# Optimization experiments

Hardware: AMD Instinct MI355X
Metric: run time of the kernel (lower is better)

## Reference

```python
import jax, jax.numpy as jnp
import numpy as np

N_NODES = 100000
N_EDGES = 3200000
BATCH = 16
LAYER_NUMBER = 4


def setup_inputs() -> dict:
    key = jax.random.key(0)
    k1, k2, k3, k4 = jax.random.split(key, 4)
    x = jax.random.normal(k1, (N_NODES, BATCH), dtype=jnp.float32)
    # learnable per-edge weights (log1p(counts) at init in the original; the
    # parameter itself is what is learned, so a plain random init is faithful)
    weights = jax.random.normal(k2, (N_EDGES,), dtype=jnp.float32)
    row = jax.random.randint(k3, (N_EDGES,), 0, N_NODES, dtype=jnp.int64)
    col = jax.random.randint(k4, (N_EDGES,), 0, N_NODES, dtype=jnp.int64)
    return {"x": x, "weights": weights, "row": row, "col": col}


def reference(x, weights, row, col):
    # Repeated sparse COO SpMM: y <- A @ y, applied layer_number times,
    # where A[row[e], col[e]] = weights[e].
    def step(y, _):
        msg = weights[:, None] * y[col]                      # [E, B] gather + scale
        y_new = jax.ops.segment_sum(msg, row, num_segments=N_NODES)  # [N, B] scatter-add
        return y_new, None

    y, _ = jax.lax.scan(step, x, None, length=LAYER_NUMBER)
    return y
```

## Files before the change

kernel.cpp:

```cpp
#include <hip/hip_runtime.h>

#define N_NODES 100000
#define N_EDGES 3200000
#define BATCH 16
#define BKT_SHIFT 6
#define BKT_NODES 64
#define K_BUCKETS 1563
#define NB 512
#define SUB (N_EDGES / NB)
#define FT 512
#define CAP 4096
#define DONE_CTR 1600
#define FLAG_CTR 1601


__global__ void zero_kernel(int* __restrict__ totals, int* __restrict__ cursor) {
    int t = threadIdx.x;
    for (int k = t; k < 2048; k += 256) totals[k] = 0;
    for (int k = t; k < K_BUCKETS; k += 256) cursor[k] = 0;
}

__global__ void __launch_bounds__(FT, 4) build_kernel(
        const int* __restrict__ row, const int* __restrict__ col,
        const float* __restrict__ w,
        int* __restrict__ totals, int* __restrict__ bptr,
        int* __restrict__ row_ptr, int* __restrict__ cursor,
        uint2* __restrict__ entries) {
    __shared__ uint2 sbuf[SUB];
    __shared__ int lbeg[K_BUCKETS];
    __shared__ int lcur[K_BUCKETS];
    __shared__ int cross[FT / 64];
    __shared__ int crossg[FT / 64];
    __shared__ int lastflag;
    int t = threadIdx.x, blk = blockIdx.x;
    int lane = t & 63, wv = t >> 6;
    int base = blk * SUB;

    for (int k = t; k < K_BUCKETS; k += FT) lcur[k] = 0;
    __syncthreads();
    for (int e = base + t; e < base + SUB; e += FT)
        atomicAdd(&lcur[row[e] >> BKT_SHIFT], 1);
    __syncthreads();

    {
        int sink = 0;
        for (int k = t; k < K_BUCKETS; k += FT) {
            int v = lcur[k];
            if (v) sink += atomicAdd(&totals[k], v);
        }
        asm volatile("" :: "v"(sink));
    }
    __syncthreads();
    if (t == 0) {
        int old = atomicAdd(&totals[DONE_CTR], 1);
        lastflag = (old == (int)gridDim.x - 1);
    }
    __syncthreads();

    if (lastflag) {
        int gloc[4];
        int gsum = 0;
        #pragma unroll
        for (int i = 0; i < 4; i++) {
            int idx = t * 4 + i;
            int v = (idx < K_BUCKETS) ? atomicAdd(&totals[idx], 0) : 0;
            gloc[i] = v;
            gsum += v;
        }
        int gpref = gsum;
        #pragma unroll
        for (int off = 1; off < 64; off <<= 1) {
            int u = __shfl_up(gpref, off, 64);
            if (lane >= off) gpref += u;
        }
        if (lane == 63) crossg[wv] = gpref;
        __syncthreads();
        int gwbase = 0;
        for (int i = 0; i < wv; i++) gwbase += crossg[i];
        int gexcl = gwbase + gpref - gsum;
        int sink = 0;
        #pragma unroll
        for (int i = 0; i < 4; i++) {
            int idx = t * 4 + i;
            if (idx < K_BUCKETS) sink += atomicExch(&bptr[idx], gexcl);
            gexcl += gloc[i];
        }
        asm volatile("" :: "v"(sink));
        __syncthreads();
        if (t == 0) {
            bptr[K_BUCKETS] = N_EDGES;
            row_ptr[N_NODES] = N_EDGES;
            int o = atomicExch(&totals[FLAG_CTR], 1);
            asm volatile("" :: "v"(o));
        }
    }

    {
        int loc[4];
        int sum = 0;
        #pragma unroll
        for (int j = 0; j < 4; j++) {
            int k = t * 4 + j;
            int v = (k < K_BUCKETS) ? lcur[k] : 0;
            loc[j] = v;
            sum += v;
        }
        int pref = sum;
        #pragma unroll
        for (int off = 1; off < 64; off <<= 1) {
            int u = __shfl_up(pref, off, 64);
            if (lane >= off) pref += u;
        }
        if (lane == 63) cross[wv] = pref;
        __syncthreads();
        int wbase = 0;
        for (int i = 0; i < wv; i++) wbase += cross[i];
        int excl = wbase + pref - sum;
        #pragma unroll
        for (int j = 0; j < 4; j++) {
            int k = t * 4 + j;
            if (k < K_BUCKETS) { lbeg[k] = excl; lcur[k] = excl; }
            excl += loc[j];
        }
    }
    __syncthreads();

    for (int e = base + t; e < base + SUB; e += FT) {
        int r = row[e];
        int bkt = r >> BKT_SHIFT;
        int pos = atomicAdd(&lcur[bkt], 1);
        sbuf[pos] = make_uint2(((unsigned)(r & (BKT_NODES - 1)) << 17) | (unsigned)col[e],
                               __float_as_uint(w[e]));
    }
    __syncthreads();

    if (!lastflag) {
        if (t == 0)
            while (atomicAdd(&totals[FLAG_CTR], 0) == 0)
                __builtin_amdgcn_s_sleep(8);
        __syncthreads();
    }

    int lane4 = t & 3;
    int sgbase = lane & ~3;
    for (int k = (t >> 2); k < K_BUCKETS; k += FT / 4) {
        int lb = lbeg[k];
        int le = lcur[k];
        int cnt = le - lb;
        int d0 = 0;
        if (lane4 == 0 && cnt > 0)
            d0 = atomicAdd(&bptr[k], 0) + atomicAdd(&cursor[k], cnt);
        d0 = __shfl(d0, sgbase, 64);
        for (int i = lb + lane4; i < le; i += 4)
            entries[d0 + (i - lb)] = sbuf[i];
    }
}

__global__ void __launch_bounds__(256) nodesort_pull1_kernel(
        const int* __restrict__ bptr, uint2* __restrict__ entries,
        int* __restrict__ row_ptr,
        const float* __restrict__ x, float* __restrict__ out) {
    __shared__ uint2 ebuf[CAP];
    __shared__ int nh[BKT_NODES];
    __shared__ int nc[BKT_NODES];
    __shared__ int nstart[BKT_NODES + 1];
    int t = threadIdx.x, b = blockIdx.x;
    int beg = bptr[b], end = bptr[b + 1];
    int n = min(end - beg, CAP);
    if (t < BKT_NODES) nh[t] = 0;
    __syncthreads();
    uint2 rs[16];
    int cnt = 0;
    #pragma unroll
    for (int i = 0; i < 16; i++) {
        int k = t + i * 256;
        if (k < n) {
            uint2 r = entries[beg + k];
            rs[i] = r;
            atomicAdd(&nh[r.x >> 17], 1);
            cnt = i + 1;
        }
    }
    __syncthreads();
    if (t < BKT_NODES) {
        int v = nh[t];
        int pref = v;
        #pragma unroll
        for (int off = 1; off < BKT_NODES; off <<= 1) {
            int u = __shfl_up(pref, off, 64);
            if (t >= off) pref += u;
        }
        int excl = pref - v;
        nstart[t] = excl;
        nc[t] = excl;
        if (t == BKT_NODES - 1) nstart[BKT_NODES] = pref;
        int node = b * BKT_NODES + t;
        if (node < N_NODES) row_ptr[node] = beg + excl;
    }
    __syncthreads();
    #pragma unroll
    for (int i = 0; i < 16; i++) {
        if (i < cnt) {
            uint2 r = rs[i];
            int pos = atomicAdd(&nc[r.x >> 17], 1);
            ebuf[pos] = r;
            entries[beg + pos] = r;
        }
    }
    __syncthreads();
    int ln = t >> 2, q = t & 3;
    int node = b * BKT_NODES + ln;
    if (node >= N_NODES) return;
    int s = nstart[ln], e = nstart[ln + 1];
    float4 acc = make_float4(0.f, 0.f, 0.f, 0.f);
    int i = s;
    while (i + 8 <= e) {
        uint2 r0 = ebuf[i + 0], r1 = ebuf[i + 1], r2 = ebuf[i + 2], r3 = ebuf[i + 3];
        uint2 r4 = ebuf[i + 4], r5 = ebuf[i + 5], r6 = ebuf[i + 6], r7 = ebuf[i + 7];
        float4 y0 = *(const float4*)&x[(r0.x & 0x1FFFFu) * BATCH + q * 4];
        float4 y1 = *(const float4*)&x[(r1.x & 0x1FFFFu) * BATCH + q * 4];
        float4 y2 = *(const float4*)&x[(r2.x & 0x1FFFFu) * BATCH + q * 4];
        float4 y3 = *(const float4*)&x[(r3.x & 0x1FFFFu) * BATCH + q * 4];
        float4 y4 = *(const float4*)&x[(r4.x & 0x1FFFFu) * BATCH + q * 4];
        float4 y5 = *(const float4*)&x[(r5.x & 0x1FFFFu) * BATCH + q * 4];
        float4 y6 = *(const float4*)&x[(r6.x & 0x1FFFFu) * BATCH + q * 4];
        float4 y7 = *(const float4*)&x[(r7.x & 0x1FFFFu) * BATCH + q * 4];
        float w0 = __uint_as_float(r0.y), w1 = __uint_as_float(r1.y);
        float w2 = __uint_as_float(r2.y), w3 = __uint_as_float(r3.y);
        float w4 = __uint_as_float(r4.y), w5 = __uint_as_float(r5.y);
        float w6 = __uint_as_float(r6.y), w7 = __uint_as_float(r7.y);
        acc.x += w0 * y0.x; acc.y += w0 * y0.y; acc.z += w0 * y0.z; acc.w += w0 * y0.w;
        acc.x += w1 * y1.x; acc.y += w1 * y1.y; acc.z += w1 * y1.z; acc.w += w1 * y1.w;
        acc.x += w2 * y2.x; acc.y += w2 * y2.y; acc.z += w2 * y2.z; acc.w += w2 * y2.w;
        acc.x += w3 * y3.x; acc.y += w3 * y3.y; acc.z += w3 * y3.z; acc.w += w3 * y3.w;
        acc.x += w4 * y4.x; acc.y += w4 * y4.y; acc.z += w4 * y4.z; acc.w += w4 * y4.w;
        acc.x += w5 * y5.x; acc.y += w5 * y5.y; acc.z += w5 * y5.z; acc.w += w5 * y5.w;
        acc.x += w6 * y6.x; acc.y += w6 * y6.y; acc.z += w6 * y6.z; acc.w += w6 * y6.w;
        acc.x += w7 * y7.x; acc.y += w7 * y7.y; acc.z += w7 * y7.z; acc.w += w7 * y7.w;
        i += 8;
    }
    for (; i < e; i++) {
        uint2 r = ebuf[i];
        float4 yv = *(const float4*)&x[(r.x & 0x1FFFFu) * BATCH + q * 4];
        float wj = __uint_as_float(r.y);
        acc.x += wj * yv.x; acc.y += wj * yv.y;
        acc.z += wj * yv.z; acc.w += wj * yv.w;
    }
    *(float4*)&out[node * BATCH + q * 4] = acc;
}

__global__ void __launch_bounds__(256) pull_kernel(const float* __restrict__ y,
                            const uint2* __restrict__ entries,
                            const int* __restrict__ row_ptr,
                            float* __restrict__ out) {
    int tid = blockIdx.x * blockDim.x + threadIdx.x;
    int node = tid >> 2;
    int q = tid & 3;
    if (node >= N_NODES) return;
    int beg = row_ptr[node];
    int end = row_ptr[node + 1];
    float4 acc = make_float4(0.f, 0.f, 0.f, 0.f);
    if (beg < end) {
        int lim = end - 1;
        uint2 r[8];
        #pragma unroll
        for (int j = 0; j < 8; j++) r[j] = entries[min(beg + j, lim)];
        int i = beg;
        while (i + 8 <= end) {
            float4 yv[8];
            #pragma unroll
            for (int j = 0; j < 8; j++)
                yv[j] = *(const float4*)&y[(r[j].x & 0x1FFFFu) * BATCH + q * 4];
            uint2 nx[8];
            #pragma unroll
            for (int j = 0; j < 8; j++)
                nx[j] = entries[min(i + 8 + j, lim)];
            #pragma unroll
            for (int j = 0; j < 8; j++) {
                float wj = __uint_as_float(r[j].y);
                acc.x += wj * yv[j].x;
                acc.y += wj * yv[j].y;
                acc.z += wj * yv[j].z;
                acc.w += wj * yv[j].w;
            }
            #pragma unroll
            for (int j = 0; j < 8; j++) r[j] = nx[j];
            i += 8;
        }
        if (i < end) {
            float4 yv[8];
            #pragma unroll
            for (int j = 0; j < 8; j++)
                yv[j] = *(const float4*)&y[(r[j].x & 0x1FFFFu) * BATCH + q * 4];
            #pragma unroll
            for (int j = 0; j < 8; j++)
                if (i + j < end) {
                    float wj = __uint_as_float(r[j].y);
                    acc.x += wj * yv[j].x;
                    acc.y += wj * yv[j].y;
                    acc.z += wj * yv[j].z;
                    acc.w += wj * yv[j].w;
                }
        }
    }
    *(float4*)&out[node * BATCH + q * 4] = acc;
}

extern "C" void kernel_launch(void* const* d_in, const int* in_sizes, int n_in,
                              void* d_out, int out_size, void* d_ws, size_t ws_size,
                              hipStream_t stream) {
    const float* x   = (const float*)d_in[0];
    const float* w   = (const float*)d_in[1];
    const int*   row = (const int*)d_in[2];
    const int*   col = (const int*)d_in[3];
    float*       out = (float*)d_out;

    char* p = (char*)d_ws;
    uint2* entries = (uint2*)p;  p += (size_t)N_EDGES * sizeof(uint2);
    float* buf     = (float*)p;  p += (size_t)N_NODES * BATCH * sizeof(float);
    int* totals  = (int*)p;      p += 8192;
    int* bptr    = (int*)p;      p += 8192;
    int* cursor  = (int*)p;      p += 8192;
    int* row_ptr = (int*)p;

    zero_kernel<<<1, 256, 0, stream>>>(totals, cursor);
    build_kernel<<<NB, FT, 0, stream>>>(row, col, w, totals, bptr, row_ptr,
                                        cursor, entries);

    nodesort_pull1_kernel<<<K_BUCKETS, 256, 0, stream>>>(bptr, entries, row_ptr, x, buf);
    const int pgrid = (N_NODES * 4 + 255) / 256;
    pull_kernel<<<pgrid, 256, 0, stream>>>(buf, entries, row_ptr, out);
    pull_kernel<<<pgrid, 256, 0, stream>>>(out, entries, row_ptr, buf);
    pull_kernel<<<pgrid, 256, 0, stream>>>(buf, entries, row_ptr, out);
}
```

Baseline: 309.8 us.

## Fuse three pull SpMM layers into one persistent kernel with grid barriers

Replaces the three back-to-back pull_kernel launches with a single mega_pull_kernel that runs all three layers. Between layers it uses a global atomic-counter barrier, and it writes intermediates with system-coherent (sc0 sc1) stores so other XCDs can see them. The row pointers are loaded once and reused across layers. This is meant to remove two launch gaps and the kernel-boundary drains. In exchange it relies on all 1563 blocks being co-resident, adds spin-wait barrier overhead, and needs an extra workspace buffer, with a fallback to the old path if the workspace is too small.

```diff
diff --git a/kernel.cpp b/kernel.cpp
--- a/kernel.cpp
+++ b/kernel.cpp
@@ -12,6 +12,10 @@
 #define CAP 4096
 #define DONE_CTR 1600
 #define FLAG_CTR 1601
+#define PULL_CTR 1700
+#define PGRID 1563
+
+typedef float v4f __attribute__((ext_vector_type(4)));
 
 
 __global__ void zero_kernel(int* __restrict__ totals, int* __restrict__ cursor) {
@@ -249,6 +253,55 @@
     *(float4*)&out[node * BATCH + q * 4] = acc;
 }
 
+__device__ __forceinline__ float4 pull_row(const float* __restrict__ y,
+        const uint2* __restrict__ entries, int beg, int end, int q) {
+    float4 acc = make_float4(0.f, 0.f, 0.f, 0.f);
+    if (beg < end) {
+        int lim = end - 1;
+        uint2 r[8];
+        #pragma unroll
+        for (int j = 0; j < 8; j++) r[j] = entries[min(beg + j, lim)];
+        int i = beg;
+        while (i + 8 <= end) {
+            float4 yv[8];
+            #pragma unroll
+            for (int j = 0; j < 8; j++)
+                yv[j] = *(const float4*)&y[(r[j].x & 0x1FFFFu) * BATCH + q * 4];
+            uint2 nx[8];
+            #pragma unroll
+            for (int j = 0; j < 8; j++)
+                nx[j] = entries[min(i + 8 + j, lim)];
+            #pragma unroll
+            for (int j = 0; j < 8; j++) {
+                float wj = __uint_as_float(r[j].y);
+                acc.x += wj * yv[j].x;
+                acc.y += wj * yv[j].y;
+                acc.z += wj * yv[j].z;
+                acc.w += wj * yv[j].w;
+            }
+            #pragma unroll
+            for (int j = 0; j < 8; j++) r[j] = nx[j];
+            i += 8;
+        }
+        if (i < end) {
+            float4 yv[8];
+            #pragma unroll
+            for (int j = 0; j < 8; j++)
+                yv[j] = *(const float4*)&y[(r[j].x & 0x1FFFFu) * BATCH + q * 4];
+            #pragma unroll
+            for (int j = 0; j < 8; j++)
+                if (i + j < end) {
+                    float wj = __uint_as_float(r[j].y);
+                    acc.x += wj * yv[j].x;
+                    acc.y += wj * yv[j].y;
+                    acc.z += wj * yv[j].z;
+                    acc.w += wj * yv[j].w;
+                }
+        }
+    }
+    return acc;
+}
+
 __global__ void __launch_bounds__(256) pull_kernel(const float* __restrict__ y,
                             const uint2* __restrict__ entries,
                             const int* __restrict__ row_ptr,
@@ -257,53 +310,50 @@
     int node = tid >> 2;
     int q = tid & 3;
     if (node >= N_NODES) return;
-    int beg = row_ptr[node];
-    int end = row_ptr[node + 1];
-    float4 acc = make_float4(0.f, 0.f, 0.f, 0.f);
-    if (beg < end) {
-        int lim = end - 1;
-        uint2 r[8];
-        #pragma unroll
-        for (int j = 0; j < 8; j++) r[j] = entries[min(beg + j, lim)];
-        int i = beg;
-        while (i + 8 <= end) {
-            float4 yv[8];
-            #pragma unroll
-            for (int j = 0; j < 8; j++)
-                yv[j] = *(const float4*)&y[(r[j].x & 0x1FFFFu) * BATCH + q * 4];
-            uint2 nx[8];
-            #pragma unroll
-            for (int j = 0; j < 8; j++)
-                nx[j] = entries[min(i + 8 + j, lim)];
-            #pragma unroll
-            for (int j = 0; j < 8; j++) {
-                float wj = __uint_as_float(r[j].y);
-                acc.x += wj * yv[j].x;
-                acc.y += wj * yv[j].y;
-                acc.z += wj * yv[j].z;
-                acc.w += wj * yv[j].w;
-            }
-            #pragma unroll
-            for (int j = 0; j < 8; j++) r[j] = nx[j];
-            i += 8;
-        }
-        if (i < end) {
-            float4 yv[8];
-            #pragma unroll
-            for (int j = 0; j < 8; j++)
-                yv[j] = *(const float4*)&y[(r[j].x & 0x1FFFFu) * BATCH + q * 4];
-            #pragma unroll
-            for (int j = 0; j < 8; j++)
-                if (i + j < end) {
-                    float wj = __uint_as_float(r[j].y);
-                    acc.x += wj * yv[j].x;
-                    acc.y += wj * yv[j].y;
-                    acc.z += wj * yv[j].z;
-                    acc.w += wj * yv[j].w;
-                }
-        }
-    }
+    float4 acc = pull_row(y, entries, row_ptr[node], row_ptr[node + 1], q);
     *(float4*)&out[node * BATCH + q * 4] = acc;
+}
+
+__device__ __forceinline__ void store_sc1(float* dst, float4 a) {
+    v4f av = {a.x, a.y, a.z, a.w};
+    asm volatile("global_store_dwordx4 %0, %1, off sc0 sc1"
+                 :: "v"(dst), "v"(av) : "memory");
+}
+
+__device__ __forceinline__ void gbar(int* ctr, int target) {
+    asm volatile("s_waitcnt vmcnt(0)" ::: "memory");
+    __syncthreads();
+    if (threadIdx.x == 0) {
+        int o = atomicAdd(ctr, 1);
+        asm volatile("" :: "v"(o));
+        while (atomicAdd(ctr, 0) < target)
+            __builtin_amdgcn_s_sleep(2);
+    }
+    __syncthreads();
+}
+
+__global__ void __launch_bounds__(256, 8) mega_pull_kernel(
+        const float* __restrict__ yin,
+        float* __restrict__ mid1,
+        float* __restrict__ mid2,
+        const uint2* __restrict__ entries,
+        const int* __restrict__ row_ptr,
+        int* __restrict__ ctr) {
+    int tid = blockIdx.x * blockDim.x + threadIdx.x;
+    int node = tid >> 2, q = tid & 3;
+    bool act = node < N_NODES;
+    int beg = 0, end = 0;
+    if (act) { beg = row_ptr[node]; end = row_ptr[node + 1]; }
+    if (act) store_sc1(&mid1[node * BATCH + q * 4],
+                       pull_row(yin, entries, beg, end, q));
+    gbar(ctr, PGRID);
+    if (act) store_sc1(&mid2[node * BATCH + q * 4],
+                       pull_row(mid1, entries, beg, end, q));
+    gbar(ctr, 2 * PGRID);
+    if (act) {
+        float4 a = pull_row(mid2, entries, beg, end, q);
+        *(float4*)&mid1[node * BATCH + q * 4] = a;
+    }
 }
 
 extern "C" void kernel_launch(void* const* d_in, const int* in_sizes, int n_in,
@@ -321,15 +371,22 @@
     int* totals  = (int*)p;      p += 8192;
     int* bptr    = (int*)p;      p += 8192;
     int* cursor  = (int*)p;      p += 8192;
-    int* row_ptr = (int*)p;
+    int* row_ptr = (int*)p;      p += 400016;
+    float* buf2  = (float*)p;
+    size_t need = (size_t)((char*)buf2 - (char*)d_ws) + (size_t)N_NODES * BATCH * sizeof(float);
 
     zero_kernel<<<1, 256, 0, stream>>>(totals, cursor);
     build_kernel<<<NB, FT, 0, stream>>>(row, col, w, totals, bptr, row_ptr,
                                         cursor, entries);
 
     nodesort_pull1_kernel<<<K_BUCKETS, 256, 0, stream>>>(bptr, entries, row_ptr, x, buf);
-    const int pgrid = (N_NODES * 4 + 255) / 256;
-    pull_kernel<<<pgrid, 256, 0, stream>>>(buf, entries, row_ptr, out);
-    pull_kernel<<<pgrid, 256, 0, stream>>>(out, entries, row_ptr, buf);
-    pull_kernel<<<pgrid, 256, 0, stream>>>(buf, entries, row_ptr, out);
-}
+
+    if (ws_size >= need) {
+        mega_pull_kernel<<<PGRID, 256, 0, stream>>>(buf, out, buf2, entries,
+                                                    row_ptr, &totals[PULL_CTR]);
+    } else {
+        pull_kernel<<<PGRID, 256, 0, stream>>>(buf, entries, row_ptr, out);
+        pull_kernel<<<PGRID, 256, 0, stream>>>(out, entries, row_ptr, buf);
+        pull_kernel<<<PGRID, 256, 0, stream>>>(buf, entries, row_ptr, out);
+    }
+}
```

Measured after the change: 628.8 us. 103% more time.
